# Kernel optimization log

Hardware: AMD Instinct MI355X
Metric: run time of the kernel (lower is better)

Reference implementation:

```python
import jax, jax.numpy as jnp
import numpy as np

POWERS = (0, 1, 2)
IN_F, OUT_F = 64, 64
B, N, T = 8, 2048, 12


def setup_inputs() -> dict:
    key = jax.random.key(0)
    ks = jax.random.split(key, 8)
    inp = {
        "x": jax.random.normal(ks[0], (B, IN_F, N, T), dtype=jnp.float32),
        "adj": jax.random.uniform(ks[1], (B, N, N), dtype=jnp.float32),
    }
    # Xavier-uniform weights per adjacency power, zero biases (as in initialize_weights)
    limit = float(np.sqrt(6.0 / (IN_F + OUT_F)))
    for i, p in enumerate(POWERS):
        inp[f"W{p}"] = jax.random.uniform(ks[2 + i], (IN_F, OUT_F), jnp.float32, -limit, limit)
        inp[f"b{p}"] = jnp.zeros((OUT_F,), jnp.float32)
    return inp


def _gcn_conv(x, adj, W, b, a_power):
    # x: [B, F, N, T]; W: [F, O]; adj: [B, N, N]
    h = jnp.einsum('bfnt,fo->bont', x, W) + b[None, :, None, None]
    # repeated diffusion along node axis: h[f, n] <- sum_m adj[n, m] h[f, m]
    for _ in range(a_power):
        h = jnp.einsum('bnm,bomt->bont', adj, h)
    return jax.nn.leaky_relu(h)  # default negative_slope 0.01, same as torch


def reference(x, adj, W0, b0, W1, b1, W2, b2):
    params = {0: (W0, b0), 1: (W1, b1), 2: (W2, b2)}
    outs = [_gcn_conv(x, adj, params[p][0], params[p][1], p) for p in POWERS]
    return jnp.concatenate(outs, axis=1)  # [B, len(POWERS)*O, N, T]
```

## Files before the change

### kernel.cpp

```cpp
#include <hip/hip_runtime.h>

#define B_ 8
#define N_ 2048
#define T_ 12
#define F_ 64
#define NT 24576
#define CH 192
#define C_ 768

typedef __bf16 bf16x8 __attribute__((ext_vector_type(8)));
typedef float f32x4 __attribute__((ext_vector_type(4)));

typedef const __attribute__((address_space(1))) unsigned int as1_uint;
typedef __attribute__((address_space(3))) unsigned int as3_uint;

__device__ __forceinline__ void gload16(const void* g, void* l) {
  __builtin_amdgcn_global_load_lds((as1_uint*)g, (as3_uint*)l, 16, 0, 0);
}

__device__ __forceinline__ unsigned short f2bf(float f) {
  unsigned int u = __float_as_uint(f);
  u += 0x7FFFu + ((u >> 16) & 1u);
  return (unsigned short)(u >> 16);
}

__device__ __forceinline__ float bf2f(unsigned short u) {
  return __uint_as_float(((unsigned int)u) << 16);
}

__device__ __forceinline__ float leaky(float v) {
  return v >= 0.0f ? v : 0.01f * v;
}

__global__ __launch_bounds__(256) void convert_rs_k(const float* __restrict__ adj,
                                                    unsigned short* __restrict__ adjb,
                                                    float* __restrict__ rs1) {
  const int row = blockIdx.x;
  const int tid = threadIdx.x;
  const int lane = tid & 63;
  const int wave = tid >> 6;
  const float4* src = reinterpret_cast<const float4*>(adj + (size_t)row * N_);
  ushort4* dst = reinterpret_cast<ushort4*>(adjb + (size_t)row * N_);

  float s = 0.0f;
#pragma unroll
  for (int i = tid; i < 512; i += 256) {
    const float4 v = src[i];
    ushort4 u;
    u.x = f2bf(v.x); u.y = f2bf(v.y); u.z = f2bf(v.z); u.w = f2bf(v.w);
    dst[i] = u;
    s += v.x + v.y + v.z + v.w;
  }
#pragma unroll
  for (int o = 32; o; o >>= 1) s += __shfl_xor(s, o);
  __shared__ float red[4];
  if (lane == 0) red[wave] = s;
  __syncthreads();
  if (tid == 0) rs1[row] = red[0] + red[1] + red[2] + red[3];
}

__global__ __launch_bounds__(256) void rs2_k(const unsigned short* __restrict__ adjb,
                                             const float* __restrict__ rs1,
                                             float* __restrict__ rs2) {
  const int row = blockIdx.x;
  const int b = row >> 11;
  const int tid = threadIdx.x;
  const int lane = tid & 63;
  const int wave = tid >> 6;
  const ushort4* src = reinterpret_cast<const ushort4*>(adjb + (size_t)row * N_);
  const float* r1 = rs1 + ((size_t)b << 11);

  float s = 0.0f;
#pragma unroll
  for (int i = tid; i < 512; i += 256) {
    const ushort4 a = src[i];
    const int m = i * 4;
    s += bf2f(a.x) * r1[m] + bf2f(a.y) * r1[m + 1]
       + bf2f(a.z) * r1[m + 2] + bf2f(a.w) * r1[m + 3];
  }
#pragma unroll
  for (int o = 32; o; o >>= 1) s += __shfl_xor(s, o);
  __shared__ float red[4];
  if (lane == 0) red[wave] = s;
  __syncthreads();
  if (tid == 0) rs2[row] = red[0] + red[1] + red[2] + red[3];
}

__global__ __launch_bounds__(256) void convertX_k(const float* __restrict__ x,
                                                  unsigned short* __restrict__ Xt) {
  __shared__ float xl[T_][260];
  const int tid = threadIdx.x;
  const int n0 = blockIdx.x * 256;
  const int f = blockIdx.y;
  const int b = blockIdx.z;

  const float* src = x + (((size_t)b * F_ + f) * N_ + n0 + tid) * T_;
  float4 v0 = *reinterpret_cast<const float4*>(src);
  float4 v1 = *reinterpret_cast<const float4*>(src + 4);
  float4 v2 = *reinterpret_cast<const float4*>(src + 8);
  xl[0][tid] = v0.x;  xl[1][tid] = v0.y;  xl[2][tid] = v0.z;  xl[3][tid] = v0.w;
  xl[4][tid] = v1.x;  xl[5][tid] = v1.y;  xl[6][tid] = v1.z;  xl[7][tid] = v1.w;
  xl[8][tid] = v2.x;  xl[9][tid] = v2.y;  xl[10][tid] = v2.z; xl[11][tid] = v2.w;
  __syncthreads();
#pragma unroll
  for (int t = 0; t < T_; ++t)
    Xt[((size_t)b * C_ + f * T_ + t) * N_ + n0 + tid] = f2bf(xl[t][tid]);
}

__device__ __forceinline__ void stage_wt(const float* __restrict__ W,
                                         unsigned short* Wt, int tid) {
  const int f = tid >> 2;
  const int q = tid & 3;
  const float4* row = reinterpret_cast<const float4*>(W + f * 64 + q * 16);
#pragma unroll
  for (int v4 = 0; v4 < 4; ++v4) {
    float4 v = row[v4];
    const int ob = q * 16 + v4 * 4;
    Wt[(ob + 0) * 72 + f] = f2bf(v.x);
    Wt[(ob + 1) * 72 + f] = f2bf(v.y);
    Wt[(ob + 2) * 72 + f] = f2bf(v.z);
    Wt[(ob + 3) * 72 + f] = f2bf(v.w);
  }
}

__global__ __launch_bounds__(256) void p0_k(const float* __restrict__ x,
                                            const float* __restrict__ W0,
                                            const float* __restrict__ bia0,
                                            float* __restrict__ out) {
  __shared__ unsigned short Wt[64 * 72];
  __shared__ float bias[64];
  const int tid = threadIdx.x;
  stage_wt(W0, Wt, tid);
  if (tid < 64) bias[tid] = bia0[tid];
  __syncthreads();

  const int lane = tid & 63;
  const int wave = tid >> 6;
  const int b = blockIdx.y;
  const int e = blockIdx.x * 64 + wave * 16 + (lane & 15);
  const int fgrp = (lane >> 4) * 8;
  const float* xb = x + (size_t)b * F_ * NT;

  bf16x8 xf[2];
#pragma unroll
  for (int kf = 0; kf < 2; ++kf)
#pragma unroll
    for (int j = 0; j < 8; ++j)
      xf[kf][j] = (__bf16)xb[(size_t)(fgrp + kf * 32 + j) * NT + e];

  float* outb = out + (size_t)b * CH * NT;
#pragma unroll
  for (int ob = 0; ob < 4; ++ob) {
    f32x4 acc = {};
#pragma unroll
    for (int kf = 0; kf < 2; ++kf) {
      bf16x8 af = *reinterpret_cast<const bf16x8*>(
          &Wt[(ob * 16 + (lane & 15)) * 72 + kf * 32 + fgrp]);
      acc = __builtin_amdgcn_mfma_f32_16x16x32_bf16(af, xf[kf], acc, 0, 0, 0);
    }
#pragma unroll
    for (int r = 0; r < 4; ++r) {
      const int o = ob * 16 + (lane >> 4) * 4 + r;
      outb[(size_t)o * NT + e] = leaky(acc[r] + bias[o]);
    }
  }
}

__global__ __launch_bounds__(256) void pT_k(const unsigned short* __restrict__ Yt,
                                            const float* __restrict__ W,
                                            const float* __restrict__ bia,
                                            const float* __restrict__ rs,
                                            float* __restrict__ out,
                                            const int ocb) {
  __shared__ unsigned short Wt[64 * 72];
  __shared__ float bias[64];
  const int tid = threadIdx.x;
  stage_wt(W, Wt, tid);
  if (tid < 64) bias[tid] = bia[tid];
  __syncthreads();

  const int lane = tid & 63;
  const int wave = tid >> 6;
  const int b = blockIdx.y;
  const int n = blockIdx.x * 16 + (lane & 15);
  const int fgrp = (lane >> 4) * 8;
  const __bf16* Yb = reinterpret_cast<const __bf16*>(Yt + (size_t)b * C_ * N_);
  const float rsv = rs[((size_t)b << 11) + n];
  float* outb = out + (size_t)b * CH * NT;

#pragma unroll
  for (int it = 0; it < 3; ++it) {
    const int t = wave * 3 + it;

    bf16x8 xf[2];
#pragma unroll
    for (int kf = 0; kf < 2; ++kf)
#pragma unroll
      for (int j = 0; j < 8; ++j)
        xf[kf][j] = Yb[(size_t)((kf * 32 + fgrp + j) * T_ + t) * N_ + n];

#pragma unroll
    for (int ob = 0; ob < 4; ++ob) {
      f32x4 acc = {};
#pragma unroll
      for (int kf = 0; kf < 2; ++kf) {
        bf16x8 af = *reinterpret_cast<const bf16x8*>(
            &Wt[(ob * 16 + (lane & 15)) * 72 + kf * 32 + fgrp]);
        acc = __builtin_amdgcn_mfma_f32_16x16x32_bf16(af, xf[kf], acc, 0, 0, 0);
      }
#pragma unroll
      for (int r = 0; r < 4; ++r) {
        const int o = ob * 16 + (lane >> 4) * 4 + r;
        outb[(size_t)(ocb + o) * NT + n * T_ + t] = leaky(acc[r] + rsv * bias[o]);
      }
    }
  }
}

__global__ __launch_bounds__(512, 2) void gemm8_k(
    const unsigned short* __restrict__ adjb,
    const unsigned short* __restrict__ Bt,
    float* __restrict__ out,
    unsigned short* __restrict__ Ht,
    const int mode, const int ochan_base)
{
  extern __shared__ __align__(16) unsigned short lds[];

  const int tid  = threadIdx.x;
  const int lane = tid & 63;
  const int wave = tid >> 6;
  const int wr = wave >> 2;
  const int wc = wave & 3;

  const int b  = blockIdx.x & 7;
  const int w  = blockIdx.x >> 3;
  const int n0 = (w & 7) * 256;
  const int c0 = (w >> 3) * 192;

  const unsigned short* A  = adjb + (size_t)b * N_ * N_;
  const unsigned short* Bm = Bt   + (size_t)b * C_ * N_;

  const int swzSrc = ((lane & 3) ^ ((lane >> 3) & 3)) * 8;
  const unsigned short* aSt1 = A + (size_t)(n0 + wave * 16 + (lane >> 2)) * N_ + swzSrc;
  const unsigned short* aSt2 = aSt1 + (size_t)128 * N_;
  const unsigned short* bSt1 = Bm + (size_t)(c0 + wave * 16 + (lane >> 2)) * N_ + swzSrc;
  const int brow2 = c0 + 128 + wave * 16 + (lane >> 2);
  const unsigned short* bSt2 = Bm + (size_t)(brow2 < C_ ? brow2 : C_ - 1) * N_ + swzSrc;
  const int ldsW = wave * 512;

  const int kg  = (lane >> 4) ^ ((lane >> 1) & 3);
  const int aRd = (wr * 128 + (lane & 15)) * 32 + kg * 8;
  const int bRd = (wc * 48  + (lane & 15)) * 32 + kg * 8;

  f32x4 acc[8][3] = {};
  bf16x8 afr[8], bfr[3];

#define STGA(LDSB, KT, KH) \
  gload16(aSt1 + (KT) * 64 + (KH) * 32, lds + (LDSB) + (KH) * 8192 + ldsW); \
  gload16(aSt2 + (KT) * 64 + (KH) * 32, lds + (LDSB) + (KH) * 8192 + ldsW + 4096);

#define STGB(LDSB, KT, KH) \
  gload16(bSt1 + (KT) * 64 + (KH) * 32, lds + (LDSB) + (KH) * 8192 + ldsW); \
  gload16(bSt2 + (KT) * 64 + (KH) * 32, lds + (LDSB) + (KH) * 8192 + ldsW + 4096);

#define RD_B(BUFB, KH) { \
  _Pragma("unroll") \
  for (int nf = 0; nf < 3; ++nf) \
    bfr[nf] = *(const bf16x8*)(lds + (BUFB) + (KH) * 8192 + nf * 512 + bRd); }

#define RD_A8(BUFA, KH) { \
  _Pragma("unroll") \
  for (int mm = 0; mm < 8; ++mm) \
    afr[mm] = *(const bf16x8*)(lds + (BUFA) + (KH) * 8192 + mm * 512 + aRd); }

#define MFMA24() { \
  _Pragma("unroll") \
  for (int mm = 0; mm < 8; ++mm) \
  _Pragma("unroll") \
  for (int nf = 0; nf < 3; ++nf) \
    acc[mm][nf] = __builtin_amdgcn_mfma_f32_16x16x32_bf16( \
        afr[mm], bfr[nf], acc[mm][nf], 0, 0, 0); }

#define MIDBAR() \
  __builtin_amdgcn_s_barrier(); \
  __builtin_amdgcn_s_setprio(1);

#define ENDBAR() \
  __builtin_amdgcn_s_setprio(0); \
  __builtin_amdgcn_s_barrier();

#define WAITV_(N) asm volatile("s_waitcnt vmcnt(" #N ")" ::: "memory");
#define WAITV(N) WAITV_(N)

  STGA(0, 0, 0)      STGB(32768, 0, 0)
  STGA(0, 0, 1)      STGB(32768, 0, 1)
  STGA(16384, 1, 0)  STGB(49152, 1, 0)
  WAITV(8)
  __builtin_amdgcn_s_barrier();

#pragma unroll 1
  for (int it = 0; it < 15; ++it) {
    const int kt0 = 2 * it;
    RD_B(32768, 0) RD_A8(0, 0)
    STGA(16384, kt0 + 1, 1) STGB(49152, kt0 + 1, 1)
    WAITV(8)
    MIDBAR() MFMA24() ENDBAR()
    RD_B(32768, 1) RD_A8(0, 1)
    STGA(0, kt0 + 2, 0) STGB(32768, kt0 + 2, 0)
    WAITV(8)
    MIDBAR() MFMA24() ENDBAR()
    RD_B(49152, 0) RD_A8(16384, 0)
    STGA(0, kt0 + 2, 1) STGB(32768, kt0 + 2, 1)
    WAITV(8)
    MIDBAR() MFMA24() ENDBAR()
    RD_B(49152, 1) RD_A8(16384, 1)
    STGA(16384, kt0 + 3, 0) STGB(49152, kt0 + 3, 0)
    WAITV(8)
    MIDBAR() MFMA24() ENDBAR()
  }

  {
    RD_B(32768, 0) RD_A8(0, 0)
    STGA(16384, 31, 1) STGB(49152, 31, 1)
    WAITV(8)
    MIDBAR() MFMA24() ENDBAR()
    RD_B(32768, 1) RD_A8(0, 1)
    WAITV(4)
    MIDBAR() MFMA24() ENDBAR()
    RD_B(49152, 0) RD_A8(16384, 0)
    WAITV(0)
    MIDBAR() MFMA24() ENDBAR()
    RD_B(49152, 1) RD_A8(16384, 1)
    MIDBAR() MFMA24()
    __builtin_amdgcn_s_setprio(0);
  }

  const int r4 = (lane >> 4) * 4;
  if (mode == 0) {
    float* outb = out + (size_t)b * CH * NT;
#pragma unroll
    for (int m = 0; m < 8; ++m) {
#pragma unroll
      for (int nf = 0; nf < 3; ++nf) {
        const int c = c0 + wc * 48 + nf * 16 + (lane & 15);
        const int o = c / 12;
        const int t = c - o * 12;
#pragma unroll
        for (int r = 0; r < 4; ++r) {
          const int n = n0 + wr * 128 + m * 16 + r4 + r;
          outb[((size_t)(ochan_base + o) * N_ + n) * T_ + t] = leaky(acc[m][nf][r]);
        }
      }
    }
  } else {
    unsigned short* Hb = Ht + (size_t)b * C_ * N_;
#pragma unroll
    for (int m = 0; m < 8; ++m) {
#pragma unroll
      for (int nf = 0; nf < 3; ++nf) {
        const int c = c0 + wc * 48 + nf * 16 + (lane & 15);
        const int nb = n0 + wr * 128 + m * 16 + r4;
        ushort4 u;
        u.x = f2bf(acc[m][nf][0]);
        u.y = f2bf(acc[m][nf][1]);
        u.z = f2bf(acc[m][nf][2]);
        u.w = f2bf(acc[m][nf][3]);
        *reinterpret_cast<ushort4*>(&Hb[(size_t)c * N_ + nb]) = u;
      }
    }
  }
#undef STGA
#undef STGB
#undef RD_B
#undef RD_A8
#undef MFMA24
#undef MIDBAR
#undef ENDBAR
#undef WAITV
#undef WAITV_
}

extern "C" void kernel_launch(void* const* d_in, const int* in_sizes, int n_in,
                              void* d_out, int out_size, void* d_ws, size_t ws_size,
                              hipStream_t stream) {
  const float* x   = (const float*)d_in[0];
  const float* adj = (const float*)d_in[1];
  const float* W0  = (const float*)d_in[2];
  const float* b0  = (const float*)d_in[3];
  const float* W1  = (const float*)d_in[4];
  const float* b1  = (const float*)d_in[5];
  const float* W2  = (const float*)d_in[6];
  const float* b2  = (const float*)d_in[7];
  float* out = (float*)d_out;

  char* ws = (char*)d_ws;
  unsigned short* adjb = (unsigned short*)ws;
  unsigned short* R1   = (unsigned short*)(ws + 67108864);
  unsigned short* R2   = (unsigned short*)(ws + 92274688);
  float* rs1 = (float*)(ws + 117440512);
  float* rs2 = (float*)(ws + 117506048);

  hipFuncSetAttribute((const void*)gemm8_k,
                      hipFuncAttributeMaxDynamicSharedMemorySize, 131072);

  hipLaunchKernelGGL(convert_rs_k, dim3(B_ * N_), dim3(256), 0, stream,
                     adj, adjb, rs1);

  hipLaunchKernelGGL(convertX_k, dim3(N_ / 256, F_, B_), dim3(256), 0, stream,
                     x, R1);

  hipLaunchKernelGGL(p0_k, dim3(NT / 64, B_), dim3(256), 0, stream,
                     x, W0, b0, out);

  hipLaunchKernelGGL(gemm8_k, dim3(256), dim3(512), 131072, stream,
                     adjb, R1, out, R2, 1, 0);

  hipLaunchKernelGGL(rs2_k, dim3(B_ * N_), dim3(256), 0, stream,
                     adjb, rs1, rs2);

  hipLaunchKernelGGL(pT_k, dim3(N_ / 16, B_), dim3(256), 0, stream,
                     R2, W1, b1, rs1, out, 64);

  hipLaunchKernelGGL(gemm8_k, dim3(256), dim3(512), 131072, stream,
                     adjb, R2, out, R1, 1, 0);

  hipLaunchKernelGGL(pT_k, dim3(N_ / 16, B_), dim3(256), 0, stream,
                     R1, W2, b2, rs2, out, 128);
}
```

Measured before the change: 268.8 us.

## Add hand-scheduled 4-stage pipelined adjacency GEMM kernel for first diffusion

Adds a new GEMM kernel that multiplies the bf16 adjacency by the transposed features. It uses a four-slot LDS ring filled by direct global-to-LDS loads, double-buffered register fragments read with inline ds_read_b128, explicit vmcnt/lgkmcnt waits, and raised wave priority around the MFMA blocks. The first diffusion launch switches to it, and its output goes straight to bf16 instead of through a mode switch. The aim is to overlap memory traffic with MFMA work and cut pipeline stalls. In exchange the hand-written waits and asm are fragile, and the second diffusion still runs the old kernel.

```diff
diff --git a/kernel.cpp b/kernel.cpp
--- a/kernel.cpp
+++ b/kernel.cpp
@@ -217,6 +217,147 @@
   }
 }
 
+__global__ __launch_bounds__(512, 2) void gemmN_k(
+    const unsigned short* __restrict__ adjb,
+    const unsigned short* __restrict__ Bt,
+    unsigned short* __restrict__ Ht)
+{
+  extern __shared__ __align__(16) unsigned short lds[];
+
+  const int tid  = threadIdx.x;
+  const int lane = tid & 63;
+  const int wave = tid >> 6;
+  const int wr = wave >> 2;
+  const int wc = wave & 3;
+
+  const int b  = blockIdx.x & 7;
+  const int w  = blockIdx.x >> 3;
+  const int n0 = (w & 7) * 256;
+  const int c0 = (w >> 3) * 192;
+
+  const unsigned short* A  = adjb + (size_t)b * N_ * N_;
+  const unsigned short* Bm = Bt   + (size_t)b * C_ * N_;
+
+  const int swzSrc = ((lane & 3) ^ ((lane >> 3) & 3)) * 8;
+  const unsigned short* aSt1 = A + (size_t)(n0 + wave * 16 + (lane >> 2)) * N_ + swzSrc;
+  const unsigned short* aSt2 = aSt1 + (size_t)128 * N_;
+  const unsigned short* bSt1 = Bm + (size_t)(c0 + wave * 16 + (lane >> 2)) * N_ + swzSrc;
+  const int brow2 = c0 + 128 + wave * 16 + (lane >> 2);
+  const unsigned short* bSt2 = Bm + (size_t)(brow2 < C_ ? brow2 : C_ - 1) * N_ + swzSrc;
+  const int ldsW = wave * 512;
+
+  const int kg  = (lane >> 4) ^ ((lane >> 1) & 3);
+  const int aRd = (wr * 128 + (lane & 15)) * 32 + kg * 8;
+  const int bRd = (wc * 48  + (lane & 15)) * 32 + kg * 8;
+
+  const unsigned aA0 = (unsigned)(uintptr_t)(lds + 0 * 16384 + aRd);
+  const unsigned aA1 = (unsigned)(uintptr_t)(lds + 1 * 16384 + aRd);
+  const unsigned aA2 = (unsigned)(uintptr_t)(lds + 2 * 16384 + aRd);
+  const unsigned aA3 = (unsigned)(uintptr_t)(lds + 3 * 16384 + aRd);
+  const unsigned bA0 = (unsigned)(uintptr_t)(lds + 0 * 16384 + 8192 + bRd);
+  const unsigned bA1 = (unsigned)(uintptr_t)(lds + 1 * 16384 + 8192 + bRd);
+  const unsigned bA2 = (unsigned)(uintptr_t)(lds + 2 * 16384 + 8192 + bRd);
+  const unsigned bA3 = (unsigned)(uintptr_t)(lds + 3 * 16384 + 8192 + bRd);
+
+  f32x4 acc[8][3] = {};
+  bf16x8 af0[8], af1[8], bf0[3], bf1[3];
+
+#define STG(S, P) \
+  gload16(aSt1 + (P) * 32, lds + (S) * 16384 + ldsW); \
+  gload16(aSt2 + (P) * 32, lds + (S) * 16384 + ldsW + 4096); \
+  gload16(bSt1 + (P) * 32, lds + (S) * 16384 + 8192 + ldsW); \
+  gload16(bSt2 + (P) * 32, lds + (S) * 16384 + 8192 + ldsW + 4096);
+
+#define DSR(D, AV, OFF) \
+  asm volatile("ds_read_b128 %0, %1 offset:" OFF : "=v"(D) : "v"(AV));
+
+#define READS(SET, AA, BA) \
+  DSR(af##SET[0], AA, "0")    DSR(af##SET[1], AA, "1024") \
+  DSR(af##SET[2], AA, "2048") DSR(af##SET[3], AA, "3072") \
+  DSR(af##SET[4], AA, "4096") DSR(af##SET[5], AA, "5120") \
+  DSR(af##SET[6], AA, "6144") DSR(af##SET[7], AA, "7168") \
+  DSR(bf##SET[0], BA, "0")    DSR(bf##SET[1], BA, "1024") \
+  DSR(bf##SET[2], BA, "2048")
+
+#define MFMA24(SET) { \
+  _Pragma("unroll") \
+  for (int mm = 0; mm < 8; ++mm) \
+  _Pragma("unroll") \
+  for (int nf = 0; nf < 3; ++nf) \
+    acc[mm][nf] = __builtin_amdgcn_mfma_f32_16x16x32_bf16( \
+        af##SET[mm], bf##SET[nf], acc[mm][nf], 0, 0, 0); }
+
+#define WAITV_(N) asm volatile("s_waitcnt vmcnt(" #N ")" ::: "memory");
+#define WAITV(N) WAITV_(N)
+
+#define PHASE(SETC, SETN, SSTG, PSTG, AAN, BAN) \
+  STG(SSTG, PSTG) \
+  WAITV(4) \
+  __builtin_amdgcn_s_barrier(); \
+  READS(SETN, AAN, BAN) \
+  asm volatile("s_waitcnt lgkmcnt(11)" ::: "memory"); \
+  __builtin_amdgcn_sched_barrier(0); \
+  __builtin_amdgcn_s_setprio(1); \
+  MFMA24(SETC) \
+  __builtin_amdgcn_s_setprio(0);
+
+  STG(0, 0)
+  STG(1, 1)
+  WAITV(4)
+  __builtin_amdgcn_s_barrier();
+  READS(0, aA0, bA0)
+  asm volatile("s_waitcnt lgkmcnt(0)" ::: "memory");
+  __builtin_amdgcn_sched_barrier(0);
+
+#pragma unroll 1
+  for (int it = 0; it < 15; ++it) {
+    const int p = 4 * it;
+    PHASE(0, 1, 2, p + 2, aA1, bA1)
+    PHASE(1, 0, 3, p + 3, aA2, bA2)
+    PHASE(0, 1, 0, p + 4, aA3, bA3)
+    PHASE(1, 0, 1, p + 5, aA0, bA0)
+  }
+  PHASE(0, 1, 2, 62, aA1, bA1)
+  PHASE(1, 0, 3, 63, aA2, bA2)
+  WAITV(0)
+  __builtin_amdgcn_s_barrier();
+  READS(1, aA3, bA3)
+  asm volatile("s_waitcnt lgkmcnt(11)" ::: "memory");
+  __builtin_amdgcn_sched_barrier(0);
+  __builtin_amdgcn_s_setprio(1);
+  MFMA24(0)
+  __builtin_amdgcn_s_setprio(0);
+  asm volatile("s_waitcnt lgkmcnt(0)" ::: "memory");
+  __builtin_amdgcn_sched_barrier(0);
+  __builtin_amdgcn_s_setprio(1);
+  MFMA24(1)
+  __builtin_amdgcn_s_setprio(0);
+
+  const int r4 = (lane >> 4) * 4;
+  unsigned short* Hb = Ht + (size_t)b * C_ * N_;
+#pragma unroll
+  for (int m = 0; m < 8; ++m) {
+#pragma unroll
+    for (int nf = 0; nf < 3; ++nf) {
+      const int c = c0 + wc * 48 + nf * 16 + (lane & 15);
+      const int nb = n0 + wr * 128 + m * 16 + r4;
+      ushort4 u;
+      u.x = f2bf(acc[m][nf][0]);
+      u.y = f2bf(acc[m][nf][1]);
+      u.z = f2bf(acc[m][nf][2]);
+      u.w = f2bf(acc[m][nf][3]);
+      *reinterpret_cast<ushort4*>(&Hb[(size_t)c * N_ + nb]) = u;
+    }
+  }
+#undef STG
+#undef DSR
+#undef READS
+#undef MFMA24
+#undef WAITV
+#undef WAITV_
+#undef PHASE
+}
+
 __global__ __launch_bounds__(512, 2) void gemm8_k(
     const unsigned short* __restrict__ adjb,
     const unsigned short* __restrict__ Bt,
@@ -402,6 +543,8 @@
 
   hipFuncSetAttribute((const void*)gemm8_k,
                       hipFuncAttributeMaxDynamicSharedMemorySize, 131072);
+  hipFuncSetAttribute((const void*)gemmN_k,
+                      hipFuncAttributeMaxDynamicSharedMemorySize, 131072);
 
   hipLaunchKernelGGL(convert_rs_k, dim3(B_ * N_), dim3(256), 0, stream,
                      adj, adjb, rs1);
@@ -412,8 +555,8 @@
   hipLaunchKernelGGL(p0_k, dim3(NT / 64, B_), dim3(256), 0, stream,
                      x, W0, b0, out);
 
-  hipLaunchKernelGGL(gemm8_k, dim3(256), dim3(512), 131072, stream,
-                     adjb, R1, out, R2, 1, 0);
+  hipLaunchKernelGGL(gemmN_k, dim3(256), dim3(512), 131072, stream,
+                     adjb, R1, R2);
 
   hipLaunchKernelGGL(rs2_k, dim3(B_ * N_), dim3(256), 0, stream,
                      adjb, rs1, rs2);
```

After: 268.9 us. No clear change (+0.0%).

## Replace large pipelined adjacency GEMM with smaller-tile single-buffered kernel

Applied to the files above, without the earlier changes.

Swaps the 256x192-tile, 512-thread, double-buffered GEMM with 128KB dynamic LDS for a 128x96-tile, 256-thread kernel with about 28KB static LDS and 1024 blocks. Each K step loads one 64-wide slice with a plain two-barrier loop instead of the hand-scheduled prefetch pipeline with priority hints. The aim is to raise occupancy and grid fill across the CUs. The cost is lower data reuse per tile, more global traffic, and no overlap between loads and MFMAs inside a block.

```diff
diff --git a/kernel.cpp b/kernel.cpp
--- a/kernel.cpp
+++ b/kernel.cpp
@@ -217,167 +217,90 @@
   }
 }
 
-__global__ __launch_bounds__(512, 2) void gemm8_k(
+__global__ __launch_bounds__(256, 4) void gemmF_k(
     const unsigned short* __restrict__ adjb,
     const unsigned short* __restrict__ Bt,
-    float* __restrict__ out,
-    unsigned short* __restrict__ Ht,
-    const int mode, const int ochan_base)
+    unsigned short* __restrict__ Ht)
 {
-  extern __shared__ __align__(16) unsigned short lds[];
+  __shared__ __align__(16) unsigned short lds[14336];
 
   const int tid  = threadIdx.x;
   const int lane = tid & 63;
   const int wave = tid >> 6;
-  const int wr = wave >> 2;
-  const int wc = wave & 3;
+  const int wm = wave >> 1;
+  const int wn = wave & 1;
 
   const int b  = blockIdx.x & 7;
-  const int w  = blockIdx.x >> 3;
-  const int n0 = (w & 7) * 256;
-  const int c0 = (w >> 3) * 192;
+  const int j  = blockIdx.x >> 3;
+  const int n0 = (j & 15) * 128;
+  const int c0 = (j >> 4) * 96;
 
   const unsigned short* A  = adjb + (size_t)b * N_ * N_;
   const unsigned short* Bm = Bt   + (size_t)b * C_ * N_;
 
-  const int swzSrc = ((lane & 3) ^ ((lane >> 3) & 3)) * 8;
-  const unsigned short* aSt1 = A + (size_t)(n0 + wave * 16 + (lane >> 2)) * N_ + swzSrc;
-  const unsigned short* aSt2 = aSt1 + (size_t)128 * N_;
-  const unsigned short* bSt1 = Bm + (size_t)(c0 + wave * 16 + (lane >> 2)) * N_ + swzSrc;
-  const int brow2 = c0 + 128 + wave * 16 + (lane >> 2);
-  const unsigned short* bSt2 = Bm + (size_t)(brow2 < C_ ? brow2 : C_ - 1) * N_ + swzSrc;
-  const int ldsW = wave * 512;
-
-  const int kg  = (lane >> 4) ^ ((lane >> 1) & 3);
-  const int aRd = (wr * 128 + (lane & 15)) * 32 + kg * 8;
-  const int bRd = (wc * 48  + (lane & 15)) * 32 + kg * 8;
-
-  f32x4 acc[8][3] = {};
-  bf16x8 afr[8], bfr[3];
-
-#define STGA(LDSB, KT, KH) \
-  gload16(aSt1 + (KT) * 64 + (KH) * 32, lds + (LDSB) + (KH) * 8192 + ldsW); \
-  gload16(aSt2 + (KT) * 64 + (KH) * 32, lds + (LDSB) + (KH) * 8192 + ldsW + 4096);
-
-#define STGB(LDSB, KT, KH) \
-  gload16(bSt1 + (KT) * 64 + (KH) * 32, lds + (LDSB) + (KH) * 8192 + ldsW); \
-  gload16(bSt2 + (KT) * 64 + (KH) * 32, lds + (LDSB) + (KH) * 8192 + ldsW + 4096);
-
-#define RD_B(BUFB, KH) { \
-  _Pragma("unroll") \
-  for (int nf = 0; nf < 3; ++nf) \
-    bfr[nf] = *(const bf16x8*)(lds + (BUFB) + (KH) * 8192 + nf * 512 + bRd); }
-
-#define RD_A8(BUFA, KH) { \
-  _Pragma("unroll") \
-  for (int mm = 0; mm < 8; ++mm) \
-    afr[mm] = *(const bf16x8*)(lds + (BUFA) + (KH) * 8192 + mm * 512 + aRd); }
-
-#define MFMA24() { \
-  _Pragma("unroll") \
-  for (int mm = 0; mm < 8; ++mm) \
-  _Pragma("unroll") \
-  for (int nf = 0; nf < 3; ++nf) \
-    acc[mm][nf] = __builtin_amdgcn_mfma_f32_16x16x32_bf16( \
-        afr[mm], bfr[nf], acc[mm][nf], 0, 0, 0); }
-
-#define MIDBAR() \
-  __builtin_amdgcn_s_barrier(); \
-  __builtin_amdgcn_s_setprio(1);
-
-#define ENDBAR() \
-  __builtin_amdgcn_s_setprio(0); \
-  __builtin_amdgcn_s_barrier();
-
-#define WAITV_(N) asm volatile("s_waitcnt vmcnt(" #N ")" ::: "memory");
-#define WAITV(N) WAITV_(N)
-
-  STGA(0, 0, 0)      STGB(32768, 0, 0)
-  STGA(0, 0, 1)      STGB(32768, 0, 1)
-  STGA(16384, 1, 0)  STGB(49152, 1, 0)
-  WAITV(8)
-  __builtin_amdgcn_s_barrier();
+  const int swz = ((lane & 7) ^ (lane >> 3)) * 8;
+  const unsigned short* aSt = A + (size_t)(n0 + wave * 32 + (lane >> 3)) * N_ + swz;
+  const unsigned short* bSt = Bm + (size_t)(c0 + wave * 24 + (lane >> 3)) * N_ + swz;
+
+  const int lr15 = lane & 15;
+  const int x7   = lane & 7;
+  const int aBase = (wm * 64 + lr15) * 64;
+  const int bBase = 8192 + (wn * 48 + lr15) * 64;
+
+  f32x4 acc[4][3] = {};
+
+#define STG(KT) \
+  gload16(aSt + (KT) * 64,            lds + wave * 2048); \
+  gload16(aSt + 8 * N_ + (KT) * 64,   lds + wave * 2048 + 512); \
+  gload16(aSt + 16 * N_ + (KT) * 64,  lds + wave * 2048 + 1024); \
+  gload16(aSt + 24 * N_ + (KT) * 64,  lds + wave * 2048 + 1536); \
+  gload16(bSt + (KT) * 64,            lds + 8192 + wave * 1536); \
+  gload16(bSt + 8 * N_ + (KT) * 64,   lds + 8192 + wave * 1536 + 512); \
+  gload16(bSt + 16 * N_ + (KT) * 64,  lds + 8192 + wave * 1536 + 1024);
+
+  STG(0)
 
 #pragma unroll 1
-  for (int it = 0; it < 15; ++it) {
-    const int kt0 = 2 * it;
-    RD_B(32768, 0) RD_A8(0, 0)
-    STGA(16384, kt0 + 1, 1) STGB(49152, kt0 + 1, 1)
-    WAITV(8)
-    MIDBAR() MFMA24() ENDBAR()
-    RD_B(32768, 1) RD_A8(0, 1)
-    STGA(0, kt0 + 2, 0) STGB(32768, kt0 + 2, 0)
-    WAITV(8)
-    MIDBAR() MFMA24() ENDBAR()
-    RD_B(49152, 0) RD_A8(16384, 0)
-    STGA(0, kt0 + 2, 1) STGB(32768, kt0 + 2, 1)
-    WAITV(8)
-    MIDBAR() MFMA24() ENDBAR()
-    RD_B(49152, 1) RD_A8(16384, 1)
-    STGA(16384, kt0 + 3, 0) STGB(49152, kt0 + 3, 0)
-    WAITV(8)
-    MIDBAR() MFMA24() ENDBAR()
-  }
-
-  {
-    RD_B(32768, 0) RD_A8(0, 0)
-    STGA(16384, 31, 1) STGB(49152, 31, 1)
-    WAITV(8)
-    MIDBAR() MFMA24() ENDBAR()
-    RD_B(32768, 1) RD_A8(0, 1)
-    WAITV(4)
-    MIDBAR() MFMA24() ENDBAR()
-    RD_B(49152, 0) RD_A8(16384, 0)
-    WAITV(0)
-    MIDBAR() MFMA24() ENDBAR()
-    RD_B(49152, 1) RD_A8(16384, 1)
-    MIDBAR() MFMA24()
-    __builtin_amdgcn_s_setprio(0);
+  for (int kt = 0; kt < 32; ++kt) {
+    __syncthreads();
+#pragma unroll
+    for (int kk = 0; kk < 2; ++kk) {
+      const int g = ((kk * 4 + (lane >> 4)) ^ x7) * 8;
+      bf16x8 af[4], bfv[3];
+#pragma unroll
+      for (int m = 0; m < 4; ++m)
+        af[m] = *(const bf16x8*)(lds + aBase + m * 1024 + g);
+#pragma unroll
+      for (int nf = 0; nf < 3; ++nf)
+        bfv[nf] = *(const bf16x8*)(lds + bBase + nf * 1024 + g);
+#pragma unroll
+      for (int m = 0; m < 4; ++m)
+#pragma unroll
+        for (int nf = 0; nf < 3; ++nf)
+          acc[m][nf] = __builtin_amdgcn_mfma_f32_16x16x32_bf16(
+              af[m], bfv[nf], acc[m][nf], 0, 0, 0);
+    }
+    __syncthreads();
+    if (kt + 1 < 32) { STG(kt + 1) }
   }
 
   const int r4 = (lane >> 4) * 4;
-  if (mode == 0) {
-    float* outb = out + (size_t)b * CH * NT;
-#pragma unroll
-    for (int m = 0; m < 8; ++m) {
-#pragma unroll
-      for (int nf = 0; nf < 3; ++nf) {
-        const int c = c0 + wc * 48 + nf * 16 + (lane & 15);
-        const int o = c / 12;
-        const int t = c - o * 12;
-#pragma unroll
-        for (int r = 0; r < 4; ++r) {
-          const int n = n0 + wr * 128 + m * 16 + r4 + r;
-          outb[((size_t)(ochan_base + o) * N_ + n) * T_ + t] = leaky(acc[m][nf][r]);
-        }
-      }
-    }
-  } else {
-    unsigned short* Hb = Ht + (size_t)b * C_ * N_;
-#pragma unroll
-    for (int m = 0; m < 8; ++m) {
-#pragma unroll
-      for (int nf = 0; nf < 3; ++nf) {
-        const int c = c0 + wc * 48 + nf * 16 + (lane & 15);
-        const int nb = n0 + wr * 128 + m * 16 + r4;
-        ushort4 u;
-        u.x = f2bf(acc[m][nf][0]);
-        u.y = f2bf(acc[m][nf][1]);
-        u.z = f2bf(acc[m][nf][2]);
-        u.w = f2bf(acc[m][nf][3]);
-        *reinterpret_cast<ushort4*>(&Hb[(size_t)c * N_ + nb]) = u;
-      }
-    }
-  }
-#undef STGA
-#undef STGB
-#undef RD_B
-#undef RD_A8
-#undef MFMA24
-#undef MIDBAR
-#undef ENDBAR
-#undef WAITV
-#undef WAITV_
+  unsigned short* Hb = Ht + (size_t)b * C_ * N_;
+#pragma unroll
+  for (int m = 0; m < 4; ++m) {
+#pragma unroll
+    for (int nf = 0; nf < 3; ++nf) {
+      const int c = c0 + wn * 48 + nf * 16 + lr15;
+      const int nb = n0 + wm * 64 + m * 16 + r4;
+      ushort4 u;
+      u.x = f2bf(acc[m][nf][0]);
+      u.y = f2bf(acc[m][nf][1]);
+      u.z = f2bf(acc[m][nf][2]);
+      u.w = f2bf(acc[m][nf][3]);
+      *reinterpret_cast<ushort4*>(&Hb[(size_t)c * N_ + nb]) = u;
+    }
+  }
+#undef STG
 }
 
 extern "C" void kernel_launch(void* const* d_in, const int* in_sizes, int n_in,
@@ -400,9 +323,6 @@
   float* rs1 = (float*)(ws + 117440512);
   float* rs2 = (float*)(ws + 117506048);
 
-  hipFuncSetAttribute((const void*)gemm8_k,
-                      hipFuncAttributeMaxDynamicSharedMemorySize, 131072);
-
   hipLaunchKernelGGL(convert_rs_k, dim3(B_ * N_), dim3(256), 0, stream,
                      adj, adjb, rs1);
 
@@ -412,8 +332,8 @@
   hipLaunchKernelGGL(p0_k, dim3(NT / 64, B_), dim3(256), 0, stream,
                      x, W0, b0, out);
 
-  hipLaunchKernelGGL(gemm8_k, dim3(256), dim3(512), 131072, stream,
-                     adjb, R1, out, R2, 1, 0);
+  hipLaunchKernelGGL(gemmF_k, dim3(1024), dim3(256), 0, stream,
+                     adjb, R1, R2);
 
   hipLaunchKernelGGL(rs2_k, dim3(B_ * N_), dim3(256), 0, stream,
                      adjb, rs1, rs2);
@@ -421,8 +341,8 @@
   hipLaunchKernelGGL(pT_k, dim3(N_ / 16, B_), dim3(256), 0, stream,
                      R2, W1, b1, rs1, out, 64);
 
-  hipLaunchKernelGGL(gemm8_k, dim3(256), dim3(512), 131072, stream,
-                     adjb, R2, out, R1, 1, 0);
+  hipLaunchKernelGGL(gemmF_k, dim3(1024), dim3(256), 0, stream,
+                     adjb, R2, R1);
 
   hipLaunchKernelGGL(pT_k, dim3(N_ / 16, B_), dim3(256), 0, stream,
                      R1, W2, b2, rs2, out, 128);
```

New measurement: 263.2 us. -2.1%, faster.

## Split GEMM k-steps into half-tile MFMA phases and reuse pT kernel for power 0

Applied to the files above, without the earlier changes.

The main adjacency GEMM loop now splits each k-step into two halves of four A fragments, interleaving the global-to-LDS staging of A and B with smaller MFMA bursts. It also adds an explicit lgkmcnt wait and a sched_barrier at each phase barrier. The goal is finer interleaving of memory traffic with compute and lower register pressure from fewer live A fragments, at the cost of twice as many barriers. Separately, the power-0 output now runs through the bf16-transposed pT kernel on R1 with a null row-sum scale, replacing the dedicated p0 kernel that read fp32 x directly.

```diff
diff --git a/kernel.cpp b/kernel.cpp
--- a/kernel.cpp
+++ b/kernel.cpp
@@ -120,49 +120,6 @@
     Wt[(ob + 1) * 72 + f] = f2bf(v.y);
     Wt[(ob + 2) * 72 + f] = f2bf(v.z);
     Wt[(ob + 3) * 72 + f] = f2bf(v.w);
-  }
-}
-
-__global__ __launch_bounds__(256) void p0_k(const float* __restrict__ x,
-                                            const float* __restrict__ W0,
-                                            const float* __restrict__ bia0,
-                                            float* __restrict__ out) {
-  __shared__ unsigned short Wt[64 * 72];
-  __shared__ float bias[64];
-  const int tid = threadIdx.x;
-  stage_wt(W0, Wt, tid);
-  if (tid < 64) bias[tid] = bia0[tid];
-  __syncthreads();
-
-  const int lane = tid & 63;
-  const int wave = tid >> 6;
-  const int b = blockIdx.y;
-  const int e = blockIdx.x * 64 + wave * 16 + (lane & 15);
-  const int fgrp = (lane >> 4) * 8;
-  const float* xb = x + (size_t)b * F_ * NT;
-
-  bf16x8 xf[2];
-#pragma unroll
-  for (int kf = 0; kf < 2; ++kf)
-#pragma unroll
-    for (int j = 0; j < 8; ++j)
-      xf[kf][j] = (__bf16)xb[(size_t)(fgrp + kf * 32 + j) * NT + e];
-
-  float* outb = out + (size_t)b * CH * NT;
-#pragma unroll
-  for (int ob = 0; ob < 4; ++ob) {
-    f32x4 acc = {};
-#pragma unroll
-    for (int kf = 0; kf < 2; ++kf) {
-      bf16x8 af = *reinterpret_cast<const bf16x8*>(
-          &Wt[(ob * 16 + (lane & 15)) * 72 + kf * 32 + fgrp]);
-      acc = __builtin_amdgcn_mfma_f32_16x16x32_bf16(af, xf[kf], acc, 0, 0, 0);
-    }
-#pragma unroll
-    for (int r = 0; r < 4; ++r) {
-      const int o = ob * 16 + (lane >> 4) * 4 + r;
-      outb[(size_t)o * NT + e] = leaky(acc[r] + bias[o]);
-    }
   }
 }
 
@@ -185,7 +142,7 @@
   const int n = blockIdx.x * 16 + (lane & 15);
   const int fgrp = (lane >> 4) * 8;
   const __bf16* Yb = reinterpret_cast<const __bf16*>(Yt + (size_t)b * C_ * N_);
-  const float rsv = rs[((size_t)b << 11) + n];
+  const float rsv = rs ? rs[((size_t)b << 11) + n] : 1.0f;
   float* outb = out + (size_t)b * CH * NT;
 
 #pragma unroll
@@ -253,7 +210,7 @@
   const int bRd = (wc * 48  + (lane & 15)) * 32 + kg * 8;
 
   f32x4 acc[8][3] = {};
-  bf16x8 afr[8], bfr[3];
+  bf16x8 afr[4], bfr[3];
 
 #define STGA(LDSB, KT, KH) \
   gload16(aSt1 + (KT) * 64 + (KH) * 32, lds + (LDSB) + (KH) * 8192 + ldsW); \
@@ -268,21 +225,23 @@
   for (int nf = 0; nf < 3; ++nf) \
     bfr[nf] = *(const bf16x8*)(lds + (BUFB) + (KH) * 8192 + nf * 512 + bRd); }
 
-#define RD_A8(BUFA, KH) { \
+#define RD_A(BUFA, KH, QM) { \
   _Pragma("unroll") \
-  for (int mm = 0; mm < 8; ++mm) \
-    afr[mm] = *(const bf16x8*)(lds + (BUFA) + (KH) * 8192 + mm * 512 + aRd); }
-
-#define MFMA24() { \
+  for (int mm = 0; mm < 4; ++mm) \
+    afr[mm] = *(const bf16x8*)(lds + (BUFA) + (KH) * 8192 + (QM) * 2048 + mm * 512 + aRd); }
+
+#define MFMA12(QM) { \
   _Pragma("unroll") \
-  for (int mm = 0; mm < 8; ++mm) \
+  for (int mm = 0; mm < 4; ++mm) \
   _Pragma("unroll") \
   for (int nf = 0; nf < 3; ++nf) \
-    acc[mm][nf] = __builtin_amdgcn_mfma_f32_16x16x32_bf16( \
-        afr[mm], bfr[nf], acc[mm][nf], 0, 0, 0); }
+    acc[(QM) * 4 + mm][nf] = __builtin_amdgcn_mfma_f32_16x16x32_bf16( \
+        afr[mm], bfr[nf], acc[(QM) * 4 + mm][nf], 0, 0, 0); }
 
 #define MIDBAR() \
   __builtin_amdgcn_s_barrier(); \
+  asm volatile("s_waitcnt lgkmcnt(0)" ::: "memory"); \
+  __builtin_amdgcn_sched_barrier(0); \
   __builtin_amdgcn_s_setprio(1);
 
 #define ENDBAR() \
@@ -301,38 +260,58 @@
 #pragma unroll 1
   for (int it = 0; it < 15; ++it) {
     const int kt0 = 2 * it;
-    RD_B(32768, 0) RD_A8(0, 0)
-    STGA(16384, kt0 + 1, 1) STGB(49152, kt0 + 1, 1)
+    RD_B(32768, 0) RD_A(0, 0, 0)
+    STGA(16384, kt0 + 1, 1)
+    MIDBAR() MFMA12(0) ENDBAR()
+    RD_A(0, 0, 1)
+    STGB(49152, kt0 + 1, 1)
     WAITV(8)
-    MIDBAR() MFMA24() ENDBAR()
-    RD_B(32768, 1) RD_A8(0, 1)
-    STGA(0, kt0 + 2, 0) STGB(32768, kt0 + 2, 0)
+    MIDBAR() MFMA12(1) ENDBAR()
+    RD_B(32768, 1) RD_A(0, 1, 0)
+    STGA(0, kt0 + 2, 0)
+    MIDBAR() MFMA12(0) ENDBAR()
+    RD_A(0, 1, 1)
+    STGB(32768, kt0 + 2, 0)
     WAITV(8)
-    MIDBAR() MFMA24() ENDBAR()
-    RD_B(49152, 0) RD_A8(16384, 0)
-    STGA(0, kt0 + 2, 1) STGB(32768, kt0 + 2, 1)
+    MIDBAR() MFMA12(1) ENDBAR()
+    RD_B(49152, 0) RD_A(16384, 0, 0)
+    STGA(0, kt0 + 2, 1)
+    MIDBAR() MFMA12(0) ENDBAR()
+    RD_A(16384, 0, 1)
+    STGB(32768, kt0 + 2, 1)
     WAITV(8)
-    MIDBAR() MFMA24() ENDBAR()
-    RD_B(49152, 1) RD_A8(16384, 1)
-    STGA(16384, kt0 + 3, 0) STGB(49152, kt0 + 3, 0)
+    MIDBAR() MFMA12(1) ENDBAR()
+    RD_B(49152, 1) RD_A(16384, 1, 0)
+    STGA(16384, kt0 + 3, 0)
+    MIDBAR() MFMA12(0) ENDBAR()
+    RD_A(16384, 1, 1)
+    STGB(49152, kt0 + 3, 0)
     WAITV(8)
-    MIDBAR() MFMA24() ENDBAR()
+    MIDBAR() MFMA12(1) ENDBAR()
   }
 
   {
-    RD_B(32768, 0) RD_A8(0, 0)
-    STGA(16384, 31, 1) STGB(49152, 31, 1)
+    RD_B(32768, 0) RD_A(0, 0, 0)
+    STGA(16384, 31, 1)
+    MIDBAR() MFMA12(0) ENDBAR()
+    RD_A(0, 0, 1)
+    STGB(49152, 31, 1)
     WAITV(8)
-    MIDBAR() MFMA24() ENDBAR()
-    RD_B(32768, 1) RD_A8(0, 1)
+    MIDBAR() MFMA12(1) ENDBAR()
+    RD_B(32768, 1) RD_A(0, 1, 0)
+    MIDBAR() MFMA12(0) ENDBAR()
+    RD_A(0, 1, 1)
     WAITV(4)
-    MIDBAR() MFMA24() ENDBAR()
-    RD_B(49152, 0) RD_A8(16384, 0)
+    MIDBAR() MFMA12(1) ENDBAR()
+    RD_B(49152, 0) RD_A(16384, 0, 0)
+    MIDBAR() MFMA12(0) ENDBAR()
+    RD_A(16384, 0, 1)
     WAITV(0)
-    MIDBAR() MFMA24() ENDBAR()
-    RD_B(49152, 1) RD_A8(16384, 1)
-    MIDBAR() MFMA24()
-    __builtin_amdgcn_s_setprio(0);
+    MIDBAR() MFMA12(1) ENDBAR()
+    RD_B(49152, 1) RD_A(16384, 1, 0)
+    MIDBAR() MFMA12(0) ENDBAR()
+    RD_A(16384, 1, 1)
+    MIDBAR() MFMA12(1) ENDBAR()
   }
 
   const int r4 = (lane >> 4) * 4;
@@ -372,8 +351,8 @@
 #undef STGA
 #undef STGB
 #undef RD_B
-#undef RD_A8
-#undef MFMA24
+#undef RD_A
+#undef MFMA12
 #undef MIDBAR
 #undef ENDBAR
 #undef WAITV
@@ -409,8 +388,8 @@
   hipLaunchKernelGGL(convertX_k, dim3(N_ / 256, F_, B_), dim3(256), 0, stream,
                      x, R1);
 
-  hipLaunchKernelGGL(p0_k, dim3(NT / 64, B_), dim3(256), 0, stream,
-                     x, W0, b0, out);
+  hipLaunchKernelGGL(pT_k, dim3(N_ / 16, B_), dim3(256), 0, stream,
+                     R1, W0, b0, (const float*)nullptr, out, 0);
 
   hipLaunchKernelGGL(gemm8_k, dim3(256), dim3(512), 131072, stream,
                      adjb, R1, out, R2, 1, 0);
```

After: 273.5 us. Within noise of the previous version (+1.7%).
